# Kernel tuning notes

Hardware: AMD Instinct MI355X
Metric: run time of the kernel (lower is better)

## Reference

```python
import jax, jax.numpy as jnp
import numpy as np

B, N, E = 4, 20000, 320000
IN_DIM, HID, OUT = 64, 128, 16


def setup_inputs() -> dict:
    key = jax.random.key(0)
    ks = jax.random.split(key, 10)
    return {
        "graph_nodes": jax.random.normal(ks[0], (B, N, IN_DIM), jnp.float32),
        "additional_features": jax.random.normal(ks[1], (B, 1), jnp.float32),
        "edge_index": jax.random.randint(ks[2], (2, E), 0, N, dtype=jnp.int32).astype(jnp.int64),
        "W1": jax.random.normal(ks[3], (IN_DIM, HID), jnp.float32) / np.sqrt(IN_DIM),
        "b1": jnp.zeros((HID,), jnp.float32),
        "W2": jax.random.normal(ks[4], (HID, HID), jnp.float32) / np.sqrt(HID),
        "b2": jnp.zeros((HID,), jnp.float32),
        "fc_w": jax.random.normal(ks[5], (HID + 1, OUT), jnp.float32) / np.sqrt(HID + 1),
        "fc_b": jnp.zeros((OUT,), jnp.float32),
        "sigma_param": jnp.zeros((OUT, 1), jnp.float32),
    }


def gcn_conv(x, src, dst, W, b, n):
    # PyG GCNConv: h = x @ W; out[dst] += deg^-1/2[src]*deg^-1/2[dst] * h[src]; out += b
    h = x @ W  # [B, N, H]
    deg = jnp.zeros((n,), h.dtype).at[dst].add(jnp.ones(dst.shape[0], h.dtype))
    dis = jax.lax.rsqrt(deg)  # self-loops guarantee deg >= 1
    norm = dis[src] * dis[dst]  # [E+N]
    msg = h[:, src, :] * norm[None, :, None]  # [B, E+N, H]
    out = jnp.zeros_like(h).at[:, dst, :].add(msg)
    return out + b


def reference(graph_nodes, additional_features, W1, b1, W2, b2, fc_w, fc_b, sigma_param, edge_index):
    n = graph_nodes.shape[1]
    loops = jnp.arange(n, dtype=edge_index.dtype)  # add_self_loops
    src = jnp.concatenate([edge_index[0], loops])
    dst = jnp.concatenate([edge_index[1], loops])
    x = jax.nn.relu(gcn_conv(graph_nodes, src, dst, W1, b1, n))
    x = jax.nn.relu(gcn_conv(x, src, dst, W2, b2, n))
    pooled = x.mean(axis=1)  # global_mean_pool (equal-size graphs)
    feats = jnp.concatenate([pooled, additional_features], axis=1)  # [B, HID+1]
    mu = feats @ fc_w + fc_b  # [B, OUT]
    sigma = jnp.exp(jnp.broadcast_to(sigma_param.reshape(1, -1), mu.shape))
    return mu, sigma
```

## Files before the change

### kernel.cpp

```cpp
#include <hip/hip_runtime.h>
#include <math.h>

#define HID 128
#define INDIM 64
#define NSH 64

typedef unsigned int uint;
typedef unsigned short ushort;
typedef __attribute__((ext_vector_type(8))) short short8;
typedef __attribute__((ext_vector_type(4))) float f32x4;

static __device__ inline float bf2f(uint h) { return __uint_as_float(h << 16); }
static __device__ inline ushort f2bf(float f) {
    uint u = __float_as_uint(f);
    return (ushort)((u + 0x7fff + ((u >> 16) & 1)) >> 16);
}
static __device__ inline uint packbf2(float a, float b) {
    return (uint)f2bf(a) | ((uint)f2bf(b) << 16);
}
static __device__ inline int imin(int a, int b) { return a < b ? a : b; }

static __device__ inline void init4(float* a, uint2 v, float sl) {
    a[0] = bf2f(v.x & 0xffffu) * sl; a[1] = bf2f(v.x >> 16) * sl;
    a[2] = bf2f(v.y & 0xffffu) * sl; a[3] = bf2f(v.y >> 16) * sl;
}
static __device__ inline void acc4(float* a, uint2 u, float f) {
    a[0] = fmaf(bf2f(u.x & 0xffffu), f, a[0]); a[1] = fmaf(bf2f(u.x >> 16), f, a[1]);
    a[2] = fmaf(bf2f(u.y & 0xffffu), f, a[2]); a[3] = fmaf(bf2f(u.y >> 16), f, a[3]);
}

__global__ __launch_bounds__(256) void k_init_cast(
    const float* __restrict__ x, const float* __restrict__ W1, const float* __restrict__ W2,
    const int* __restrict__ ei,
    uint* __restrict__ xbf, uint* __restrict__ w1t, uint* __restrict__ w2t,
    int* cnt, float* pooledS, int* flag, int N)
{
    int gid = blockIdx.x * 256 + threadIdx.x;
    int stride = gridDim.x * 256;
    if (blockIdx.x == 0) {
        __shared__ int sbad;
        if (threadIdx.x == 0) sbad = 0;
        __syncthreads();
        int bad = (ei[2 * threadIdx.x + 1] != 0) ? 1 : 0;
        if (__any(bad) && (threadIdx.x & 63) == 0) atomicOr(&sbad, 1);
        __syncthreads();
        if (threadIdx.x == 0) *flag = sbad;
    }
    int total = N * 128;
    for (int i = gid; i < total; i += stride) {
        int n = i >> 7, r = i & 127;
        int b = r >> 5, c2 = r & 31;
        const float* s = x + ((size_t)b * N + n) * 64 + c2 * 2;
        xbf[i] = packbf2(s[0], s[1]);
    }
    if (gid < 128 * 32) { int c = gid >> 5, k2 = gid & 31; w1t[gid] = packbf2(W1[(2 * k2) * 128 + c], W1[(2 * k2 + 1) * 128 + c]); }
    if (gid < 128 * 64) { int c = gid >> 6, k2 = gid & 63; w2t[gid] = packbf2(W2[(2 * k2) * 128 + c], W2[(2 * k2 + 1) * 128 + c]); }
    if (gid < N) cnt[gid] = 0;
    if (gid < NSH * 512) pooledS[gid] = 0.f;
}

__global__ __launch_bounds__(256) void k_edges(const int* __restrict__ ei, const int* __restrict__ flag,
                                               int* __restrict__ src, int* __restrict__ dst,
                                               int* cnt, int E) {
    int e = blockIdx.x * 256 + threadIdx.x;
    if (e >= E) return;
    int s, d;
    if (*flag) { s = ei[e]; d = ei[(size_t)E + e]; }
    else       { s = ei[2 * (size_t)e]; d = ei[2 * (size_t)E + 2 * (size_t)e]; }
    src[e] = s; dst[e] = d;
    atomicAdd(&cnt[d], 1);
}

__global__ __launch_bounds__(1024) void k_scan(const int* __restrict__ cnt, int* __restrict__ row_ptr,
                                               float* __restrict__ dis, int* __restrict__ fillcnt, int N) {
    __shared__ int wsum[16];
    int t = threadIdx.x;
    int chunk = (N + 1023) >> 10;
    int lo = t * chunk; if (lo > N) lo = N;
    int hi = lo + chunk; if (hi > N) hi = N;
    int s = 0;
#pragma unroll 4
    for (int i = lo; i < hi; i++) s += cnt[i];
    int lane = t & 63, wid = t >> 6;
    int v = s;
#pragma unroll
    for (int d = 1; d < 64; d <<= 1) {
        int u = __shfl_up(v, d);
        if (lane >= d) v += u;
    }
    if (lane == 63) wsum[wid] = v;
    __syncthreads();
    if (wid == 0) {
        int wv = (lane < 16) ? wsum[lane] : 0;
#pragma unroll
        for (int d = 1; d < 16; d <<= 1) {
            int u = __shfl_up(wv, d);
            if (lane >= d) wv += u;
        }
        if (lane < 16) wsum[lane] = wv;
    }
    __syncthreads();
    int base = (wid > 0 ? wsum[wid - 1] : 0) + (v - s);
    int acc = base;
#pragma unroll 4
    for (int i = lo; i < hi; i++) {
        row_ptr[i] = acc;
        int c = cnt[i];
        acc += c;
        dis[i] = rsqrtf((float)(c + 1));
        fillcnt[i] = 0;
    }
    if (t == 0) row_ptr[N] = wsum[15];
}

__global__ __launch_bounds__(256) void k_fill(const int* __restrict__ src, const int* __restrict__ dst,
                                              const int* __restrict__ row_ptr, int* fillcnt,
                                              int* __restrict__ col, float* __restrict__ wsrc,
                                              const float* __restrict__ dis, int E) {
    int e = blockIdx.x * 256 + threadIdx.x;
    if (e >= E) return;
    int d = dst[e], s = src[e];
    int p = row_ptr[d] + atomicAdd(&fillcnt[d], 1);
    col[p] = s;
    wsrc[p] = dis[s];
}

__global__ __launch_bounds__(256, 4) void k_l1(
    const uint* __restrict__ xbf, const int* __restrict__ rp, const int* __restrict__ col,
    const float* __restrict__ wsrc, const float* __restrict__ dis,
    const uint* __restrict__ w1t, const float* __restrict__ b1,
    uint* __restrict__ x1, int N, int ntile)
{
    __shared__ __align__(16) char sW[16384];
    __shared__ __align__(16) char sXa[4][2048];
    int t = threadIdx.x, w = t >> 6, l = t & 63;
    int g = l >> 4, row = l & 15;
    for (int i = t; i < 1024; i += 256) {
        int c = i >> 3, ch = i & 7;
        *(uint4*)(sW + c * 128 + ((ch ^ (c & 7)) << 4)) = *(const uint4*)(w1t + c * 32 + ch * 4);
    }
    __syncthreads();
    int tile = blockIdx.x * 4 + w;
    if (tile >= ntile) return;
    char* sX = sXa[w];
    const uint2* xr = (const uint2*)xbf;

    int n0 = tile * 4;
    int r0 = rp[n0], r1 = rp[n0 + 1], r2 = rp[n0 + 2], r3 = rp[n0 + 3], r4 = rp[n0 + 4];
    int e0 = r0, e1 = r1, e2 = r2, e3 = r3;
    float dn0 = dis[n0], dn1 = dis[n0 + 1], dn2 = dis[n0 + 2], dn3 = dis[n0 + 3];
    float ac0[4], ac1[4], ac2[4], ac3[4];
    init4(ac0, xr[(size_t)n0 * 64 + l], dn0 * dn0);
    init4(ac1, xr[(size_t)(n0 + 1) * 64 + l], dn1 * dn1);
    init4(ac2, xr[(size_t)(n0 + 2) * 64 + l], dn2 * dn2);
    init4(ac3, xr[(size_t)(n0 + 3) * 64 + l], dn3 * dn3);

#define A2(j) do { \
    int c0_ = col[e##j], c1_ = col[e##j + 1]; \
    float f0_ = wsrc[e##j] * dn##j, f1_ = wsrc[e##j + 1] * dn##j; \
    uint2 u0_ = xr[(size_t)c0_ * 64 + l], u1_ = xr[(size_t)c1_ * 64 + l]; \
    acc4(ac##j, u0_, f0_); acc4(ac##j, u1_, f1_); e##j += 2; } while (0)
#define A1(j) do { \
    int c0_ = col[e##j]; float f0_ = wsrc[e##j] * dn##j; \
    uint2 u0_ = xr[(size_t)c0_ * 64 + l]; acc4(ac##j, u0_, f0_); e##j += 1; } while (0)

    int m = imin(imin(r1 - e0, r2 - e1), imin(r3 - e2, r4 - e3)) >> 1;
    for (int it = 0; it < m; it++) { A2(0); A2(1); A2(2); A2(3); }
    int p01 = imin(r1 - e0, r2 - e1) >> 1;
    for (int it = 0; it < p01; it++) { A2(0); A2(1); }
    int p23 = imin(r3 - e2, r4 - e3) >> 1;
    for (int it = 0; it < p23; it++) { A2(2); A2(3); }
    while (e0 + 1 < r1) A2(0);
    if (e0 < r1) A1(0);
    while (e1 + 1 < r2) A2(1);
    if (e1 < r2) A1(1);
    while (e2 + 1 < r3) A2(2);
    if (e2 < r3) A1(2);
    while (e3 + 1 < r4) A2(3);
    if (e3 < r4) A1(3);
#undef A2
#undef A1

    {
        uint2 pk;
        pk.x = packbf2(ac0[0], ac0[1]); pk.y = packbf2(ac0[2], ac0[3]);
        int wr = g;
        *(uint2*)(sX + wr * 128 + (((row >> 1) ^ (wr & 7)) << 4) + ((row & 1) << 3)) = pk;
        pk.x = packbf2(ac1[0], ac1[1]); pk.y = packbf2(ac1[2], ac1[3]);
        wr = 4 + g;
        *(uint2*)(sX + wr * 128 + (((row >> 1) ^ (wr & 7)) << 4) + ((row & 1) << 3)) = pk;
        pk.x = packbf2(ac2[0], ac2[1]); pk.y = packbf2(ac2[2], ac2[3]);
        wr = 8 + g;
        *(uint2*)(sX + wr * 128 + (((row >> 1) ^ (wr & 7)) << 4) + ((row & 1) << 3)) = pk;
        pk.x = packbf2(ac3[0], ac3[1]); pk.y = packbf2(ac3[2], ac3[3]);
        wr = 12 + g;
        *(uint2*)(sX + wr * 128 + (((row >> 1) ^ (wr & 7)) << 4) + ((row & 1) << 3)) = pk;
    }
    int ro0 = row * 128 + ((g ^ (row & 7)) << 4);
    int ro1 = row * 128 + (((4 + g) ^ (row & 7)) << 4);
    short8 xf0 = *(const short8*)(sX + ro0);
    short8 xf1 = *(const short8*)(sX + ro1);
    int nodeL = row >> 2, bb = row & 3;
    size_t rnew = ((size_t)bb * N + (size_t)tile * 4 + nodeL) * 32;
#pragma unroll
    for (int q = 0; q < 8; q++) {
        f32x4 a = {0.f, 0.f, 0.f, 0.f};
        const char* wb = sW + q * 2048;
        a = __builtin_amdgcn_mfma_f32_16x16x32_bf16(*(const short8*)(wb + ro0), xf0, a, 0, 0, 0);
        a = __builtin_amdgcn_mfma_f32_16x16x32_bf16(*(const short8*)(wb + ro1), xf1, a, 0, 0, 0);
        float4 bbv = *(const float4*)(b1 + q * 16 + g * 4);
        uint2 o;
        o.x = packbf2(fmaxf(a.x + bbv.x, 0.f), fmaxf(a.y + bbv.y, 0.f));
        o.y = packbf2(fmaxf(a.z + bbv.z, 0.f), fmaxf(a.w + bbv.w, 0.f));
        ((uint2*)x1)[rnew + q * 4 + g] = o;
    }
}

#define BATCH_MAP() \
    int bid = blockIdx.x; \
    int bq = (bid & 7) >> 1; \
    int jj = ((bid >> 3) << 1) | (bid & 1); \
    int tl = jj * 4 + w; \
    if (tl >= ntiles) return;

__global__ __launch_bounds__(256, 6) void k_l2(
    const uint* __restrict__ x1, const int* __restrict__ rp, const int* __restrict__ col,
    const float* __restrict__ wsrc, const float* __restrict__ dis,
    const uint* __restrict__ w2t, const float* __restrict__ b2,
    float* __restrict__ pooledS, int N, int ntiles, float invN)
{
    __shared__ __align__(16) char sXa[4][4096];
    int t = threadIdx.x, w = t >> 6, l = t & 63;
    int g = l >> 4, row = l & 15;
    BATCH_MAP();
    char* sX = sXa[w];
    const uint* xb = x1 + (size_t)bq * N * 64;
    int n0 = tl * 16;
    int lofs = (((l >> 2) ^ 99) & 0);  (void)lofs;

    for (int p = 0; p < 16; p++) {
        int node = n0 + p;
        float dn = dis[node];
        int beg = rp[node], end = rp[node + 1];
        uint v = xb[(size_t)node * 64 + l];
        float sl = dn * dn;
        float a0 = bf2f(v & 0xffffu) * sl, a1 = bf2f(v >> 16) * sl;
        int e = beg;
        for (; e + 3 < end; e += 4) {
            int s0 = col[e], s1 = col[e + 1], s2 = col[e + 2], s3 = col[e + 3];
            float f0 = wsrc[e] * dn, f1 = wsrc[e + 1] * dn;
            float f2 = wsrc[e + 2] * dn, f3 = wsrc[e + 3] * dn;
            uint u0 = xb[(size_t)s0 * 64 + l];
            uint u1 = xb[(size_t)s1 * 64 + l];
            uint u2 = xb[(size_t)s2 * 64 + l];
            uint u3 = xb[(size_t)s3 * 64 + l];
            a0 = fmaf(bf2f(u0 & 0xffffu), f0, a0); a1 = fmaf(bf2f(u0 >> 16), f0, a1);
            a0 = fmaf(bf2f(u1 & 0xffffu), f1, a0); a1 = fmaf(bf2f(u1 >> 16), f1, a1);
            a0 = fmaf(bf2f(u2 & 0xffffu), f2, a0); a1 = fmaf(bf2f(u2 >> 16), f2, a1);
            a0 = fmaf(bf2f(u3 & 0xffffu), f3, a0); a1 = fmaf(bf2f(u3 >> 16), f3, a1);
        }
        for (; e < end; e++) {
            int s = col[e];
            float f = wsrc[e] * dn;
            uint u = xb[(size_t)s * 64 + l];
            a0 = fmaf(bf2f(u & 0xffffu), f, a0); a1 = fmaf(bf2f(u >> 16), f, a1);
        }
        *(uint*)(sX + p * 256 + ((((l >> 2) ^ (p & 7))) << 4) + ((l & 3) << 2)) = packbf2(a0, a1);
    }
    short8 xf[4];
#pragma unroll
    for (int ks = 0; ks < 4; ks++)
        xf[ks] = *(const short8*)(sX + row * 256 + (((ks * 4 + g) ^ (row & 7)) << 4));
    int sh = tl & (NSH - 1);
    float* pd = pooledS + (size_t)sh * 512 + bq * 128;
#pragma unroll 2
    for (int q = 0; q < 8; q++) {
        const uint* wq = w2t + (q * 16 + row) * 64 + g * 4;
        f32x4 a = {0.f, 0.f, 0.f, 0.f};
        a = __builtin_amdgcn_mfma_f32_16x16x32_bf16(*(const short8*)(wq),      xf[0], a, 0, 0, 0);
        a = __builtin_amdgcn_mfma_f32_16x16x32_bf16(*(const short8*)(wq + 16), xf[1], a, 0, 0, 0);
        a = __builtin_amdgcn_mfma_f32_16x16x32_bf16(*(const short8*)(wq + 32), xf[2], a, 0, 0, 0);
        a = __builtin_amdgcn_mfma_f32_16x16x32_bf16(*(const short8*)(wq + 48), xf[3], a, 0, 0, 0);
        float4 bb = *(const float4*)(b2 + q * 16 + g * 4);
        float v0 = fmaxf(a.x + bb.x, 0.f);
        float v1 = fmaxf(a.y + bb.y, 0.f);
        float v2 = fmaxf(a.z + bb.z, 0.f);
        float v3 = fmaxf(a.w + bb.w, 0.f);
        v0 += __shfl_xor(v0, 1); v0 += __shfl_xor(v0, 2); v0 += __shfl_xor(v0, 4); v0 += __shfl_xor(v0, 8);
        v1 += __shfl_xor(v1, 1); v1 += __shfl_xor(v1, 2); v1 += __shfl_xor(v1, 4); v1 += __shfl_xor(v1, 8);
        v2 += __shfl_xor(v2, 1); v2 += __shfl_xor(v2, 2); v2 += __shfl_xor(v2, 4); v2 += __shfl_xor(v2, 8);
        v3 += __shfl_xor(v3, 1); v3 += __shfl_xor(v3, 2); v3 += __shfl_xor(v3, 4); v3 += __shfl_xor(v3, 8);
        if (row == 0) {
            atomicAdd(&pd[q * 16 + g * 4 + 0], v0 * invN);
            atomicAdd(&pd[q * 16 + g * 4 + 1], v1 * invN);
            atomicAdd(&pd[q * 16 + g * 4 + 2], v2 * invN);
            atomicAdd(&pd[q * 16 + g * 4 + 3], v3 * invN);
        }
    }
}

__global__ __launch_bounds__(512) void k_head(const float* __restrict__ pooledS, const float* __restrict__ af,
                                              const float* __restrict__ fcw, const float* __restrict__ fcb,
                                              const float* __restrict__ sig, float* __restrict__ out, int B) {
    __shared__ float pool[512];
    int t = threadIdx.x;
    float s = 0.f;
#pragma unroll 8
    for (int sh = 0; sh < NSH; sh++) s += pooledS[sh * 512 + t];
    pool[t] = s;
    __syncthreads();
    if (t >= B * 16) return;
    int b = t >> 4, o = t & 15;
    float acc = fcb[o];
    for (int c = 0; c < HID; c++) acc = fmaf(pool[b * 128 + c], fcw[c * 16 + o], acc);
    acc = fmaf(af[b], fcw[HID * 16 + o], acc);
    out[t] = acc;
    out[B * 16 + t] = expf(sig[o]);
}


extern "C" void kernel_launch(void* const* d_in, const int* in_sizes, int n_in,
                              void* d_out, int out_size, void* d_ws, size_t ws_size,
                              hipStream_t stream) {
    const float* x   = (const float*)d_in[0];
    const float* af  = (const float*)d_in[1];
    const int*   ei  = (const int*)d_in[2];
    const float* W1  = (const float*)d_in[3];
    const float* b1  = (const float*)d_in[4];
    const float* W2  = (const float*)d_in[5];
    const float* b2  = (const float*)d_in[6];
    const float* fcw = (const float*)d_in[7];
    const float* fcb = (const float*)d_in[8];
    const float* sig = (const float*)d_in[9];

    int B = in_sizes[1];
    int E = in_sizes[2] / 2;
    int N = in_sizes[0] / (B * INDIM);
    int ntile1 = N / 4;
    int ntiles2 = N / 16;

    char* p = (char*)d_ws;
    auto alloc = [&](size_t bytes) { void* r = (void*)p; p += (bytes + 255) & ~(size_t)255; return r; };
    int*    cnt     = (int*)alloc((size_t)N * 4);
    int*    fillcnt = (int*)alloc((size_t)N * 4);
    int*    row_ptr = (int*)alloc((size_t)(N + 1) * 4);
    int*    colA    = (int*)alloc((size_t)E * 4);
    int*    srcA    = (int*)alloc((size_t)E * 4);
    int*    dstA    = (int*)alloc((size_t)E * 4);
    float*  wsrcA   = (float*)alloc((size_t)E * 4);
    float*  dis     = (float*)alloc((size_t)N * 4);
    float*  pooledS = (float*)alloc((size_t)NSH * 512 * 4);
    int*    flag    = (int*)alloc(256);
    uint*   xbf     = (uint*)alloc((size_t)N * 128 * 4);
    uint*   x1      = (uint*)alloc((size_t)N * 4 * 64 * 4);
    uint*   w1t     = (uint*)alloc((size_t)128 * 32 * 4);
    uint*   w2t     = (uint*)alloc((size_t)128 * 64 * 4);
    (void)ws_size;

    int gE = (E + 255) / 256;
    int gL1 = (ntile1 + 3) / 4;
    int gL2 = 8 * ((((ntiles2 + 3) / 4) + 1) / 2);

    k_init_cast<<<2048, 256, 0, stream>>>(x, W1, W2, ei, xbf, w1t, w2t, cnt, pooledS, flag, N);
    k_edges<<<gE, 256, 0, stream>>>(ei, flag, srcA, dstA, cnt, E);
    k_scan<<<1, 1024, 0, stream>>>(cnt, row_ptr, dis, fillcnt, N);
    k_fill<<<gE, 256, 0, stream>>>(srcA, dstA, row_ptr, fillcnt, colA, wsrcA, dis, E);

    k_l1<<<gL1, 256, 0, stream>>>(xbf, row_ptr, colA, wsrcA, dis, w1t, b1, x1, N, ntile1);
    k_l2<<<gL2, 256, 0, stream>>>(x1, row_ptr, colA, wsrcA, dis, w2t, b2, pooledS, N, ntiles2, 1.0f / (float)N);

    k_head<<<1, 512, 0, stream>>>(pooledS, af, fcw, fcb, sig, (float*)d_out, B);
}
```

Baseline: 190.4 us.

## Interleave batch features per node so layer-2 gather loads all batches at once

```diff
diff --git a/kernel.cpp b/kernel.cpp
--- a/kernel.cpp
+++ b/kernel.cpp
@@ -20,6 +20,18 @@
 }
 static __device__ inline int imin(int a, int b) { return a < b ? a : b; }
 
+static __device__ inline void init8(float* a, uint4 v, float sl) {
+    a[0] = bf2f(v.x & 0xffffu) * sl; a[1] = bf2f(v.x >> 16) * sl;
+    a[2] = bf2f(v.y & 0xffffu) * sl; a[3] = bf2f(v.y >> 16) * sl;
+    a[4] = bf2f(v.z & 0xffffu) * sl; a[5] = bf2f(v.z >> 16) * sl;
+    a[6] = bf2f(v.w & 0xffffu) * sl; a[7] = bf2f(v.w >> 16) * sl;
+}
+static __device__ inline void acc8(float* a, uint4 u, float f) {
+    a[0] = fmaf(bf2f(u.x & 0xffffu), f, a[0]); a[1] = fmaf(bf2f(u.x >> 16), f, a[1]);
+    a[2] = fmaf(bf2f(u.y & 0xffffu), f, a[2]); a[3] = fmaf(bf2f(u.y >> 16), f, a[3]);
+    a[4] = fmaf(bf2f(u.z & 0xffffu), f, a[4]); a[5] = fmaf(bf2f(u.z >> 16), f, a[5]);
+    a[6] = fmaf(bf2f(u.w & 0xffffu), f, a[6]); a[7] = fmaf(bf2f(u.w >> 16), f, a[7]);
+}
 static __device__ inline void init4(float* a, uint2 v, float sl) {
     a[0] = bf2f(v.x & 0xffffu) * sl; a[1] = bf2f(v.x >> 16) * sl;
     a[2] = bf2f(v.y & 0xffffu) * sl; a[3] = bf2f(v.y >> 16) * sl;
@@ -200,79 +212,75 @@
     int ro1 = row * 128 + (((4 + g) ^ (row & 7)) << 4);
     short8 xf0 = *(const short8*)(sX + ro0);
     short8 xf1 = *(const short8*)(sX + ro1);
-    int nodeL = row >> 2, bb = row & 3;
-    size_t rnew = ((size_t)bb * N + (size_t)tile * 4 + nodeL) * 32;
+    size_t rbase = ((size_t)tile * 16 + row) * 32;
 #pragma unroll
     for (int q = 0; q < 8; q++) {
         f32x4 a = {0.f, 0.f, 0.f, 0.f};
         const char* wb = sW + q * 2048;
         a = __builtin_amdgcn_mfma_f32_16x16x32_bf16(*(const short8*)(wb + ro0), xf0, a, 0, 0, 0);
         a = __builtin_amdgcn_mfma_f32_16x16x32_bf16(*(const short8*)(wb + ro1), xf1, a, 0, 0, 0);
-        float4 bbv = *(const float4*)(b1 + q * 16 + g * 4);
+        float4 bb = *(const float4*)(b1 + q * 16 + g * 4);
         uint2 o;
-        o.x = packbf2(fmaxf(a.x + bbv.x, 0.f), fmaxf(a.y + bbv.y, 0.f));
-        o.y = packbf2(fmaxf(a.z + bbv.z, 0.f), fmaxf(a.w + bbv.w, 0.f));
-        ((uint2*)x1)[rnew + q * 4 + g] = o;
-    }
-}
-
-#define BATCH_MAP() \
-    int bid = blockIdx.x; \
-    int bq = (bid & 7) >> 1; \
-    int jj = ((bid >> 3) << 1) | (bid & 1); \
-    int tl = jj * 4 + w; \
-    if (tl >= ntiles) return;
+        o.x = packbf2(fmaxf(a.x + bb.x, 0.f), fmaxf(a.y + bb.y, 0.f));
+        o.y = packbf2(fmaxf(a.z + bb.z, 0.f), fmaxf(a.w + bb.w, 0.f));
+        ((uint2*)x1)[rbase + q * 4 + g] = o;
+    }
+}
 
 __global__ __launch_bounds__(256, 6) void k_l2(
     const uint* __restrict__ x1, const int* __restrict__ rp, const int* __restrict__ col,
     const float* __restrict__ wsrc, const float* __restrict__ dis,
     const uint* __restrict__ w2t, const float* __restrict__ b2,
-    float* __restrict__ pooledS, int N, int ntiles, float invN)
+    float* __restrict__ pooledS, int N, int ntile, float invN)
 {
     __shared__ __align__(16) char sXa[4][4096];
     int t = threadIdx.x, w = t >> 6, l = t & 63;
     int g = l >> 4, row = l & 15;
-    BATCH_MAP();
+    int tile = blockIdx.x * 4 + w;
+    if (tile >= ntile) return;
     char* sX = sXa[w];
-    const uint* xb = x1 + (size_t)bq * N * 64;
-    int n0 = tl * 16;
-    int lofs = (((l >> 2) ^ 99) & 0);  (void)lofs;
-
-    for (int p = 0; p < 16; p++) {
-        int node = n0 + p;
-        float dn = dis[node];
-        int beg = rp[node], end = rp[node + 1];
-        uint v = xb[(size_t)node * 64 + l];
-        float sl = dn * dn;
-        float a0 = bf2f(v & 0xffffu) * sl, a1 = bf2f(v >> 16) * sl;
+    const uint4* xr = (const uint4*)x1;
+    int n0 = tile * 4;
+
+#pragma unroll
+    for (int p = 0; p < 4; p++) {
+        int n = n0 + p;
+        float dn = dis[n];
+        int beg = rp[n], end = rp[n + 1];
+        float ac[8];
+        init8(ac, xr[(size_t)n * 64 + l], dn * dn);
         int e = beg;
         for (; e + 3 < end; e += 4) {
             int s0 = col[e], s1 = col[e + 1], s2 = col[e + 2], s3 = col[e + 3];
             float f0 = wsrc[e] * dn, f1 = wsrc[e + 1] * dn;
             float f2 = wsrc[e + 2] * dn, f3 = wsrc[e + 3] * dn;
-            uint u0 = xb[(size_t)s0 * 64 + l];
-            uint u1 = xb[(size_t)s1 * 64 + l];
-            uint u2 = xb[(size_t)s2 * 64 + l];
-            uint u3 = xb[(size_t)s3 * 64 + l];
-            a0 = fmaf(bf2f(u0 & 0xffffu), f0, a0); a1 = fmaf(bf2f(u0 >> 16), f0, a1);
-            a0 = fmaf(bf2f(u1 & 0xffffu), f1, a0); a1 = fmaf(bf2f(u1 >> 16), f1, a1);
-            a0 = fmaf(bf2f(u2 & 0xffffu), f2, a0); a1 = fmaf(bf2f(u2 >> 16), f2, a1);
-            a0 = fmaf(bf2f(u3 & 0xffffu), f3, a0); a1 = fmaf(bf2f(u3 >> 16), f3, a1);
+            uint4 u0 = xr[(size_t)s0 * 64 + l];
+            uint4 u1 = xr[(size_t)s1 * 64 + l];
+            uint4 u2 = xr[(size_t)s2 * 64 + l];
+            uint4 u3 = xr[(size_t)s3 * 64 + l];
+            acc8(ac, u0, f0);
+            acc8(ac, u1, f1);
+            acc8(ac, u2, f2);
+            acc8(ac, u3, f3);
         }
         for (; e < end; e++) {
             int s = col[e];
             float f = wsrc[e] * dn;
-            uint u = xb[(size_t)s * 64 + l];
-            a0 = fmaf(bf2f(u & 0xffffu), f, a0); a1 = fmaf(bf2f(u >> 16), f, a1);
+            uint4 u = xr[(size_t)s * 64 + l];
+            acc8(ac, u, f);
         }
-        *(uint*)(sX + p * 256 + ((((l >> 2) ^ (p & 7))) << 4) + ((l & 3) << 2)) = packbf2(a0, a1);
+        int wr = p * 4 + g;
+        uint4 pk;
+        pk.x = packbf2(ac[0], ac[1]); pk.y = packbf2(ac[2], ac[3]);
+        pk.z = packbf2(ac[4], ac[5]); pk.w = packbf2(ac[6], ac[7]);
+        *(uint4*)(sX + wr * 256 + ((row ^ (wr & 7)) << 4)) = pk;
     }
     short8 xf[4];
 #pragma unroll
     for (int ks = 0; ks < 4; ks++)
         xf[ks] = *(const short8*)(sX + row * 256 + (((ks * 4 + g) ^ (row & 7)) << 4));
-    int sh = tl & (NSH - 1);
-    float* pd = pooledS + (size_t)sh * 512 + bq * 128;
+    int sh = tile & (NSH - 1);
+    float* pd0 = pooledS + (size_t)sh * 512;
 #pragma unroll 2
     for (int q = 0; q < 8; q++) {
         const uint* wq = w2t + (q * 16 + row) * 64 + g * 4;
@@ -286,15 +294,16 @@
         float v1 = fmaxf(a.y + bb.y, 0.f);
         float v2 = fmaxf(a.z + bb.z, 0.f);
         float v3 = fmaxf(a.w + bb.w, 0.f);
-        v0 += __shfl_xor(v0, 1); v0 += __shfl_xor(v0, 2); v0 += __shfl_xor(v0, 4); v0 += __shfl_xor(v0, 8);
-        v1 += __shfl_xor(v1, 1); v1 += __shfl_xor(v1, 2); v1 += __shfl_xor(v1, 4); v1 += __shfl_xor(v1, 8);
-        v2 += __shfl_xor(v2, 1); v2 += __shfl_xor(v2, 2); v2 += __shfl_xor(v2, 4); v2 += __shfl_xor(v2, 8);
-        v3 += __shfl_xor(v3, 1); v3 += __shfl_xor(v3, 2); v3 += __shfl_xor(v3, 4); v3 += __shfl_xor(v3, 8);
-        if (row == 0) {
-            atomicAdd(&pd[q * 16 + g * 4 + 0], v0 * invN);
-            atomicAdd(&pd[q * 16 + g * 4 + 1], v1 * invN);
-            atomicAdd(&pd[q * 16 + g * 4 + 2], v2 * invN);
-            atomicAdd(&pd[q * 16 + g * 4 + 3], v3 * invN);
+        v0 += __shfl_xor(v0, 4); v0 += __shfl_xor(v0, 8);
+        v1 += __shfl_xor(v1, 4); v1 += __shfl_xor(v1, 8);
+        v2 += __shfl_xor(v2, 4); v2 += __shfl_xor(v2, 8);
+        v3 += __shfl_xor(v3, 4); v3 += __shfl_xor(v3, 8);
+        if ((l & 12) == 0) {
+            float* pd = pd0 + (l & 3) * 128 + q * 16 + g * 4;
+            atomicAdd(pd + 0, v0 * invN);
+            atomicAdd(pd + 1, v1 * invN);
+            atomicAdd(pd + 2, v2 * invN);
+            atomicAdd(pd + 3, v3 * invN);
         }
     }
 }
@@ -336,8 +345,7 @@
     int B = in_sizes[1];
     int E = in_sizes[2] / 2;
     int N = in_sizes[0] / (B * INDIM);
-    int ntile1 = N / 4;
-    int ntiles2 = N / 16;
+    int ntile = N / 4;
 
     char* p = (char*)d_ws;
     auto alloc = [&](size_t bytes) { void* r = (void*)p; p += (bytes + 255) & ~(size_t)255; return r; };
@@ -358,16 +366,15 @@
     (void)ws_size;
 
     int gE = (E + 255) / 256;
-    int gL1 = (ntile1 + 3) / 4;
-    int gL2 = 8 * ((((ntiles2 + 3) / 4) + 1) / 2);
+    int gL = (ntile + 3) / 4;
 
     k_init_cast<<<2048, 256, 0, stream>>>(x, W1, W2, ei, xbf, w1t, w2t, cnt, pooledS, flag, N);
     k_edges<<<gE, 256, 0, stream>>>(ei, flag, srcA, dstA, cnt, E);
     k_scan<<<1, 1024, 0, stream>>>(cnt, row_ptr, dis, fillcnt, N);
     k_fill<<<gE, 256, 0, stream>>>(srcA, dstA, row_ptr, fillcnt, colA, wsrcA, dis, E);
 
-    k_l1<<<gL1, 256, 0, stream>>>(xbf, row_ptr, colA, wsrcA, dis, w1t, b1, x1, N, ntile1);
-    k_l2<<<gL2, 256, 0, stream>>>(x1, row_ptr, colA, wsrcA, dis, w2t, b2, pooledS, N, ntiles2, 1.0f / (float)N);
+    k_l1<<<gL, 256, 0, stream>>>(xbf, row_ptr, colA, wsrcA, dis, w1t, b1, x1, N, ntile);
+    k_l2<<<gL, 256, 0, stream>>>(x1, row_ptr, colA, wsrcA, dis, w2t, b2, pooledS, N, ntile, 1.0f / (float)N);
 
     k_head<<<1, 512, 0, stream>>>(pooledS, af, fcw, fcb, sig, (float*)d_out, B);
 }
```

After: 181.4 us. 1.05x faster.
